# Kernel optimization log

Hardware: AMD Instinct MI355X
Metric: run time of the kernel (lower is better)

Reference implementation:

```python
import jax, jax.numpy as jnp
import numpy as np

N = 8192        # num_nodes
H = 128         # h_dim
E = 131072      # num edges (avg degree 16)
NREL = 90       # num relations
NB = 8          # num_bases (block-diagonal decomposition)
SI = H // NB    # block size 16


def setup_inputs() -> dict:
    key = jax.random.key(0)
    ks = jax.random.split(key, 24)
    sc = 0.01
    n = lambda k, shape, s=sc: jax.random.normal(k, shape, dtype=jnp.float32) * s
    return {
        'node_ids': jnp.arange(N, dtype=jnp.int32),
        'src': jax.random.randint(ks[0], (E,), 0, N, dtype=jnp.int32),
        'dst': jax.random.randint(ks[1], (E,), 0, N, dtype=jnp.int32),
        'etypes': jax.random.randint(ks[2], (E,), 0, NREL, dtype=jnp.int32),
        'norm': jax.random.uniform(ks[3], (E, 1), dtype=jnp.float32),
        'eps': jax.random.normal(ks[4], (N, H), dtype=jnp.float32),
        # input embedding layer
        'embedding': n(ks[5], (N, H)),
        # RelGraphConv layer 0 ('bdd'): per-relation block-diag weights, self-loop, bias
        'W0': n(ks[6], (NREL, NB, SI, SI)),
        'loop0': n(ks[7], (H, H)),
        'b0': jnp.zeros((H,), jnp.float32),
        # RelGraphConv layer 1
        'W1': n(ks[8], (NREL, NB, SI, SI)),
        'loop1': n(ks[9], (H, H)),
        'b1': jnp.zeros((H,), jnp.float32),
        # z_layer: Linear(H, 2H)  (weights stored as (in, out))
        'Wz': n(ks[10], (H, 2 * H)),
        'bz': jnp.zeros((2 * H,), jnp.float32),
        # inter_layer (UpdateLayer): Linear(H, H) + h_bias
        'Wi': n(ks[11], (H, H)),
        'bi': jnp.zeros((H,), jnp.float32),
        'hbi': jnp.zeros((H,), jnp.float32),
        # output_layer (second UpdateLayer)
        'Wo': n(ks[12], (H, H)),
        'bo': jnp.zeros((H,), jnp.float32),
        'hbo': jnp.zeros((H,), jnp.float32),
    }


def _rgcn_bdd(h, W, loop_w, bias, src, dst, etypes, norm, act):
    # gather src features, split into NB blocks of size SI
    x = h[src].reshape(-1, NB, SI)                       # [E, NB, SI]
    Wg = W[etypes]                                       # [E, NB, SI, SI] per-edge relation block weights
    msg = jnp.einsum('ebi,ebio->ebo', x, Wg).reshape(-1, H) * norm  # [E, H]
    agg = jax.ops.segment_sum(msg, dst, num_segments=N)  # scatter-add to dst
    out = agg + bias + h @ loop_w                        # self-loop + bias
    return act(out) if act is not None else out


def reference(node_ids, src, dst, etypes, norm, eps, embedding,
              W0, loop0, b0, W1, loop1, b1,
              Wz, bz, Wi, bi, hbi, Wo, bo, hbo):
    # input layer: embedding lookup; saved as input_embed
    x0 = embedding[node_ids]                             # [N, H]
    h = _rgcn_bdd(x0, W0, loop0, b0, src, dst, etypes, norm, jax.nn.relu)
    h = _rgcn_bdd(h, W1, loop1, b1, src, dst, etypes, norm, None)
    # VAE head: z ~ N(mean, exp(log_std))
    zml = h @ Wz + bz                                    # [N, 2H]
    z_mean, z_log_std = jnp.split(zml, 2, axis=-1)
    z = z_mean + jnp.exp(z_log_std) * eps                # reparameterized sample
    # decode 1: outer-product reconstruction + fused update
    R = z @ z.T                                          # [N, N]
    h = R @ (z @ Wi + bi) + R @ x0 + hbi
    # decode 2
    R2 = h @ h.T                                         # [N, N]
    out = R2 @ (h @ Wo + bo) + R2 @ x0 + hbo
    return out
```

## Files before the change

### kernel.cpp

```cpp
#include <hip/hip_runtime.h>
#include <hip/hip_bf16.h>
#include <math.h>

#define Hdim 128
#define NBq 8
#define SIq 16
#define LDP 136
#define SKX 64

typedef __attribute__((ext_vector_type(8))) short short8x;
typedef __attribute__((ext_vector_type(8))) _Float16 half8x;
typedef __attribute__((ext_vector_type(4))) float f32x4;
typedef __attribute__((ext_vector_type(4))) unsigned short ushort4x;
typedef __attribute__((ext_vector_type(2))) _Float16 half2x;

__device__ inline unsigned short f2b(float f) {
  unsigned int u = __float_as_uint(f);
  return (unsigned short)((u + 0x7fffu + ((u >> 16) & 1u)) >> 16);
}
__device__ inline unsigned int pack2(float lo, float hi) {
  return (unsigned int)f2b(lo) | ((unsigned int)f2b(hi) << 16);
}
__device__ inline unsigned short f2h(float f) {
  _Float16 h = (_Float16)f;
  unsigned short u;
  __builtin_memcpy(&u, &h, 2);
  return u;
}
__device__ inline half2x u2h(unsigned int u) {
  union { unsigned int u; half2x h; } v;
  v.u = u;
  return v.h;
}

__global__ __launch_bounds__(256) void k_pre(
    const float* __restrict__ emb, const int* __restrict__ ids, float* __restrict__ x0,
    unsigned short* __restrict__ x0h, unsigned short* __restrict__ x0t, int Nn,
    const float* __restrict__ W0, unsigned short* __restrict__ Wt0,
    const float* __restrict__ W1, unsigned short* __restrict__ Wt1, int w0elems,
    const float* __restrict__ l0, const float* __restrict__ l1,
    const float* __restrict__ Wi, const float* __restrict__ Wo, const float* __restrict__ Wz,
    unsigned short* __restrict__ l0t, unsigned short* __restrict__ l1t,
    unsigned short* __restrict__ Wit, unsigned short* __restrict__ Wot,
    unsigned short* __restrict__ Wzt,
    const int* __restrict__ dst, int* __restrict__ cnt, int E,
    int b1, int b2, int b3) {
  int bx = blockIdx.x, t = threadIdx.x;
  if (bx < b1) {
    int idx = bx * 256 + t;
    int n = idx >> 5, c4 = idx & 31;
    int s = ids[n];
    float4 v = ((const float4*)emb)[(size_t)s * 32 + c4];
    ((float4*)x0)[(size_t)n * 32 + c4] = v;
    ushort4x h;
    h.x = f2h(v.x); h.y = f2h(v.y); h.z = f2h(v.z); h.w = f2h(v.w);
    ((ushort4x*)x0h)[(size_t)n * 32 + c4] = h;
    int c0 = c4 * 4;
    x0t[(size_t)(c0 + 0) * Nn + n] = h.x;
    x0t[(size_t)(c0 + 1) * Nn + n] = h.y;
    x0t[(size_t)(c0 + 2) * Nn + n] = h.z;
    x0t[(size_t)(c0 + 3) * Nn + n] = h.w;
  } else if (bx < b2) {
    int idx = (bx - b1) * 256 + t;
    const float* W = (idx < w0elems) ? W0 : W1;
    unsigned short* Wt = (idx < w0elems) ? Wt0 : Wt1;
    int local = (idx < w0elems) ? idx : idx - w0elems;
    int rb = local >> 8, io = local & 255;
    int i = io >> 4, o = io & 15;
    Wt[(size_t)rb * 256 + o * 16 + i] = f2h(W[(size_t)rb * 256 + i * 16 + o]);
  } else if (bx < b3) {
    int idx = (bx - b2) * 256 + t;
    if (idx < 65536) {
      int w = idx >> 14, local = idx & 16383;
      const float* in = (w == 0) ? l0 : (w == 1) ? l1 : (w == 2) ? Wi : Wo;
      unsigned short* out = (w == 0) ? l0t : (w == 1) ? l1t : (w == 2) ? Wit : Wot;
      int n = local >> 7, k = local & 127;
      out[local] = f2b(in[k * 128 + n]);
    } else {
      int local = idx - 65536;
      int n = local >> 7, k = local & 127;
      Wzt[local] = f2b(Wz[k * 256 + n]);
    }
  } else {
    int e = (bx - b3) * 256 + t;
    if (e < E) atomicAdd(&cnt[dst[e]], 1);
  }
}

__global__ __launch_bounds__(1024) void k_scan(const int* __restrict__ cnt,
                                               int* __restrict__ off,
                                               int* __restrict__ cur, int N, int E) {
  __shared__ int part[1024];
  int t = threadIdx.x;
  int ipt = N / 1024;
  int base = t * ipt;
  int loc[8];
  int s = 0;
  for (int i = 0; i < ipt; ++i) { loc[i] = s; s += cnt[base + i]; }
  part[t] = s;
  __syncthreads();
  for (int d = 1; d < 1024; d <<= 1) {
    int v = part[t];
    int add = (t >= d) ? part[t - d] : 0;
    __syncthreads();
    part[t] = v + add;
    __syncthreads();
  }
  int pre = (t == 0) ? 0 : part[t - 1];
  for (int i = 0; i < ipt; ++i) {
    int o = pre + loc[i];
    off[base + i] = o;
    cur[base + i] = o;
  }
  if (t == 0) off[N] = E;
}

__global__ void k_scatter(const int* __restrict__ src, const int* __restrict__ dst,
                          const int* __restrict__ et, const float* __restrict__ norm,
                          int* __restrict__ cur, int4* __restrict__ pedge, int E) {
  int e = blockIdx.x * blockDim.x + threadIdx.x;
  if (e >= E) return;
  int p = atomicAdd(&cur[dst[e]], 1);
  pedge[p] = make_int4(src[e], et[e], __float_as_int(norm[e]), 0);
}

__global__ __launch_bounds__(128) void k_edge(
    const unsigned short* __restrict__ xh, const unsigned short* __restrict__ Wt,
    const int* __restrict__ off, const int4* __restrict__ pedge,
    float* __restrict__ agg) {
  int n = blockIdx.x;
  int f = threadIdx.x;
  int b = f >> 4, o = f & 15;
  int j0 = off[n], j1 = off[n + 1];
  float acc = 0.f;
#pragma unroll 2
  for (int j = j0; j < j1; ++j) {
    int4 meta = pedge[j];
    int s = meta.x;
    int r = meta.y;
    float nv = __int_as_float(meta.z);
    const uint4* xp = (const uint4*)(xh + (size_t)s * Hdim + b * SIq);
    const uint4* wp = (const uint4*)(Wt + ((size_t)r * NBq + b) * 256 + o * SIq);
    uint4 xa = xp[0], xc = xp[1];
    uint4 wa = wp[0], wc = wp[1];
#if __has_builtin(__builtin_amdgcn_fdot2)
    float d0 = 0.f, d1 = 0.f;
    d0 = __builtin_amdgcn_fdot2(u2h(xa.x), u2h(wa.x), d0, false);
    d1 = __builtin_amdgcn_fdot2(u2h(xa.y), u2h(wa.y), d1, false);
    d0 = __builtin_amdgcn_fdot2(u2h(xa.z), u2h(wa.z), d0, false);
    d1 = __builtin_amdgcn_fdot2(u2h(xa.w), u2h(wa.w), d1, false);
    d0 = __builtin_amdgcn_fdot2(u2h(xc.x), u2h(wc.x), d0, false);
    d1 = __builtin_amdgcn_fdot2(u2h(xc.y), u2h(wc.y), d1, false);
    d0 = __builtin_amdgcn_fdot2(u2h(xc.z), u2h(wc.z), d0, false);
    d1 = __builtin_amdgcn_fdot2(u2h(xc.w), u2h(wc.w), d1, false);
    acc = fmaf(d0 + d1, nv, acc);
#else
    float d = 0.f;
    unsigned int xu[8] = {xa.x, xa.y, xa.z, xa.w, xc.x, xc.y, xc.z, xc.w};
    unsigned int wu[8] = {wa.x, wa.y, wa.z, wa.w, wc.x, wc.y, wc.z, wc.w};
#pragma unroll
    for (int k = 0; k < 8; ++k) {
      half2x xv = u2h(xu[k]), wv = u2h(wu[k]);
      d += (float)xv.x * (float)wv.x + (float)xv.y * (float)wv.y;
    }
    acc = fmaf(d, nv, acc);
#endif
  }
  agg[(size_t)n * Hdim + f] = acc;
}

__global__ __launch_bounds__(256) void k_bgemm(
    const float* __restrict__ A, const unsigned short* __restrict__ Bt,
    float* __restrict__ C,
    const float* __restrict__ addm, const float* __restrict__ bias,
    int M, int Nc, int relu, unsigned short* __restrict__ Ch) {
  __shared__ unsigned short Al[32][136];
  __shared__ unsigned short Bl[64][136];
  int t = threadIdx.x;
  int bm = blockIdx.x * 32, bn = blockIdx.y * 64;
  {
    int r = t >> 3, c0 = (t & 7) << 4;
    const float4* ap = (const float4*)(A + (size_t)(bm + r) * Hdim + c0);
    float4 a0 = ap[0], a1 = ap[1], a2 = ap[2], a3 = ap[3];
    uint4 p0 = { pack2(a0.x, a0.y), pack2(a0.z, a0.w), pack2(a1.x, a1.y), pack2(a1.z, a1.w) };
    uint4 p1 = { pack2(a2.x, a2.y), pack2(a2.z, a2.w), pack2(a3.x, a3.y), pack2(a3.z, a3.w) };
    *(uint4*)&Al[r][c0]     = p0;
    *(uint4*)&Al[r][c0 + 8] = p1;
  }
  {
    int n = t >> 2, k0 = (t & 3) << 5;
    const uint4* bp = (const uint4*)(Bt + (size_t)(bn + n) * Hdim + k0);
    uint4 b0 = bp[0], b1 = bp[1], b2 = bp[2], b3 = bp[3];
    *(uint4*)&Bl[n][k0]      = b0;
    *(uint4*)&Bl[n][k0 + 8]  = b1;
    *(uint4*)&Bl[n][k0 + 16] = b2;
    *(uint4*)&Bl[n][k0 + 24] = b3;
  }
  __syncthreads();
  int wv = t >> 6, ln = t & 63;
  int mt = wv & 1;
  int nt0 = (wv >> 1) << 1;
  int lm = ln & 15, lk = ln >> 4;
  f32x4 acc0 = {0.f, 0.f, 0.f, 0.f}, acc1 = {0.f, 0.f, 0.f, 0.f};
#pragma unroll
  for (int ks = 0; ks < 4; ++ks) {
    short8x af = *(const short8x*)&Al[mt * 16 + lm][ks * 32 + lk * 8];
    short8x bf0 = *(const short8x*)&Bl[nt0 * 16 + lm][ks * 32 + lk * 8];
    short8x bf1 = *(const short8x*)&Bl[(nt0 + 1) * 16 + lm][ks * 32 + lk * 8];
    acc0 = __builtin_amdgcn_mfma_f32_16x16x32_bf16(af, bf0, acc0, 0, 0, 0);
    acc1 = __builtin_amdgcn_mfma_f32_16x16x32_bf16(af, bf1, acc1, 0, 0, 0);
  }
  int gcol0 = bn + nt0 * 16 + lm;
  int gcol1 = gcol0 + 16;
  float b0v = bias ? bias[gcol0] : 0.f;
  float b1v = bias ? bias[gcol1] : 0.f;
#pragma unroll
  for (int reg = 0; reg < 4; ++reg) {
    int grow = bm + mt * 16 + lk * 4 + reg;
    size_t o0 = (size_t)grow * Nc + gcol0;
    size_t o1 = (size_t)grow * Nc + gcol1;
    float v0 = acc0[reg] + b0v;
    float v1 = acc1[reg] + b1v;
    if (addm) { v0 += addm[o0]; v1 += addm[o1]; }
    if (relu) { v0 = fmaxf(v0, 0.f); v1 = fmaxf(v1, 0.f); }
    C[o0] = v0;
    C[o1] = v1;
    if (Ch) { Ch[o0] = f2h(v0); Ch[o1] = f2h(v1); }
  }
}

__global__ __launch_bounds__(256) void k_bgemm_z(
    const float* __restrict__ A, const unsigned short* __restrict__ Wzt,
    const float* __restrict__ bz, const float* __restrict__ eps,
    float* __restrict__ Z, int M, int Nn,
    unsigned short* __restrict__ Zth, float* __restrict__ gz) {
  __shared__ unsigned short Al[32][136];
  __shared__ unsigned short Bm[64][136];
  __shared__ unsigned short Bl[64][136];
  int t = threadIdx.x;
  int bm = blockIdx.x * 32, bn = blockIdx.y * 64;
  if (gz && blockIdx.x == 0 && blockIdx.y == 0 && t < 64)
    ((float4*)gz)[t] = make_float4(0.f, 0.f, 0.f, 0.f);
  {
    int r = t >> 3, c0 = (t & 7) << 4;
    const float4* ap = (const float4*)(A + (size_t)(bm + r) * Hdim + c0);
    float4 a0 = ap[0], a1 = ap[1], a2 = ap[2], a3 = ap[3];
    uint4 p0 = { pack2(a0.x, a0.y), pack2(a0.z, a0.w), pack2(a1.x, a1.y), pack2(a1.z, a1.w) };
    uint4 p1 = { pack2(a2.x, a2.y), pack2(a2.z, a2.w), pack2(a3.x, a3.y), pack2(a3.z, a3.w) };
    *(uint4*)&Al[r][c0]     = p0;
    *(uint4*)&Al[r][c0 + 8] = p1;
  }
  {
    int n = t >> 2, k0 = (t & 3) << 5;
    const uint4* mp = (const uint4*)(Wzt + (size_t)(bn + n) * Hdim + k0);
    const uint4* lp = (const uint4*)(Wzt + (size_t)(bn + 128 + n) * Hdim + k0);
    uint4 m0 = mp[0], m1 = mp[1], m2 = mp[2], m3 = mp[3];
    uint4 l0 = lp[0], l1 = lp[1], l2 = lp[2], l3 = lp[3];
    *(uint4*)&Bm[n][k0]      = m0; *(uint4*)&Bm[n][k0 + 8]  = m1;
    *(uint4*)&Bm[n][k0 + 16] = m2; *(uint4*)&Bm[n][k0 + 24] = m3;
    *(uint4*)&Bl[n][k0]      = l0; *(uint4*)&Bl[n][k0 + 8]  = l1;
    *(uint4*)&Bl[n][k0 + 16] = l2; *(uint4*)&Bl[n][k0 + 24] = l3;
  }
  __syncthreads();
  int wv = t >> 6, ln = t & 63;
  int mt = wv & 1;
  int nt0 = (wv >> 1) << 1;
  int lm = ln & 15, lk = ln >> 4;
  f32x4 am0 = {0,0,0,0}, am1 = {0,0,0,0}, al0 = {0,0,0,0}, al1 = {0,0,0,0};
#pragma unroll
  for (int ks = 0; ks < 4; ++ks) {
    short8x af = *(const short8x*)&Al[mt * 16 + lm][ks * 32 + lk * 8];
    short8x bm0 = *(const short8x*)&Bm[nt0 * 16 + lm][ks * 32 + lk * 8];
    short8x bm1 = *(const short8x*)&Bm[(nt0 + 1) * 16 + lm][ks * 32 + lk * 8];
    short8x bl0 = *(const short8x*)&Bl[nt0 * 16 + lm][ks * 32 + lk * 8];
    short8x bl1 = *(const short8x*)&Bl[(nt0 + 1) * 16 + lm][ks * 32 + lk * 8];
    am0 = __builtin_amdgcn_mfma_f32_16x16x32_bf16(af, bm0, am0, 0, 0, 0);
    am1 = __builtin_amdgcn_mfma_f32_16x16x32_bf16(af, bm1, am1, 0, 0, 0);
    al0 = __builtin_amdgcn_mfma_f32_16x16x32_bf16(af, bl0, al0, 0, 0, 0);
    al1 = __builtin_amdgcn_mfma_f32_16x16x32_bf16(af, bl1, al1, 0, 0, 0);
  }
  int gcol0 = bn + nt0 * 16 + lm;
  int gcol1 = gcol0 + 16;
  float bm0v = bz[gcol0], bm1v = bz[gcol1];
  float bl0v = bz[128 + gcol0], bl1v = bz[128 + gcol1];
#pragma unroll
  for (int reg = 0; reg < 4; ++reg) {
    int grow = bm + mt * 16 + lk * 4 + reg;
    size_t o0 = (size_t)grow * Hdim + gcol0;
    size_t o1 = (size_t)grow * Hdim + gcol1;
    float v0 = am0[reg] + bm0v + expf(al0[reg] + bl0v) * eps[o0];
    float v1 = am1[reg] + bm1v + expf(al1[reg] + bl1v) * eps[o1];
    Z[o0] = v0;
    Z[o1] = v1;
    Zth[(size_t)gcol0 * Nn + grow] = f2h(v0);
    Zth[(size_t)gcol1 * Nn + grow] = f2h(v1);
  }
}

__global__ __launch_bounds__(256) void k_xty2m(
    const unsigned short* __restrict__ Zt, const unsigned short* __restrict__ X0t,
    float* __restrict__ part, float* __restrict__ s1, float* __restrict__ cx0, int N) {
  int kc = blockIdx.x, yt = blockIdx.y;
  int t = threadIdx.x;
  int KC = N / SKX;
  int k0 = kc * KC;
  if (yt == 4) {
    int c = t & 127;
    const unsigned short* row = ((t >> 7) ? X0t : Zt) + (size_t)c * N + k0;
    float acc = 0.f;
    for (int i = 0; i < KC; i += 8) {
      uint4 v = *(const uint4*)(row + i);
      half2x a0 = u2h(v.x), a1 = u2h(v.y), a2 = u2h(v.z), a3 = u2h(v.w);
      acc += (float)a0.x + (float)a0.y + (float)a1.x + (float)a1.y
           + (float)a2.x + (float)a2.y + (float)a3.x + (float)a3.y;
    }
    atomicAdd(((t >> 7) ? cx0 : s1) + c, acc);
    return;
  }
  __shared__ unsigned short Asl[128][72];
  __shared__ unsigned short Bsl[64][72];
  int wv = t >> 6, ln = t & 63, lm = ln & 15, lk = ln >> 4;
  f32x4 acc[8];
#pragma unroll
  for (int i = 0; i < 8; ++i) acc[i] = (f32x4){0.f, 0.f, 0.f, 0.f};
  for (int ch = 0; ch < KC; ch += 64) {
    {
      int r = t >> 1, s = (t & 1) * 32;
      const uint4* gp = (const uint4*)(Zt + (size_t)r * N + k0 + ch + s);
      uint4 v0 = gp[0], v1 = gp[1], v2 = gp[2], v3 = gp[3];
      *(uint4*)&Asl[r][s]      = v0;
      *(uint4*)&Asl[r][s + 8]  = v1;
      *(uint4*)&Asl[r][s + 16] = v2;
      *(uint4*)&Asl[r][s + 24] = v3;
    }
    if (t < 128) {
      int n = t >> 1, s = (t & 1) * 32;
      int yn = yt * 64 + n;
      const unsigned short* Sb = (yn < 128) ? (Zt + (size_t)yn * N)
                                            : (X0t + (size_t)(yn - 128) * N);
      const uint4* gp = (const uint4*)(Sb + k0 + ch + s);
      uint4 v0 = gp[0], v1 = gp[1], v2 = gp[2], v3 = gp[3];
      *(uint4*)&Bsl[n][s]      = v0;
      *(uint4*)&Bsl[n][s + 8]  = v1;
      *(uint4*)&Bsl[n][s + 16] = v2;
      *(uint4*)&Bsl[n][s + 24] = v3;
    }
    __syncthreads();
#pragma unroll
    for (int ks = 0; ks < 2; ++ks) {
      half8x bf = *(const half8x*)&Bsl[wv * 16 + lm][ks * 32 + lk * 8];
#pragma unroll
      for (int mi = 0; mi < 8; ++mi) {
        half8x af = *(const half8x*)&Asl[mi * 16 + lm][ks * 32 + lk * 8];
        acc[mi] = __builtin_amdgcn_mfma_f32_16x16x32_f16(af, bf, acc[mi], 0, 0, 0);
      }
    }
    __syncthreads();
  }
  int gcol = yt * 64 + wv * 16 + lm;
  float* pb = part + (size_t)kc * (128 * 256) + gcol;
#pragma unroll
  for (int mi = 0; mi < 8; ++mi)
#pragma unroll
    for (int rg = 0; rg < 4; ++rg)
      pb[(size_t)(mi * 16 + lk * 4 + rg) * 256] = acc[mi][rg];
}

__global__ __launch_bounds__(256) void k_red(const float* __restrict__ part,
                                             float* __restrict__ SP) {
  int idx = blockIdx.x * 256 + threadIdx.x;
  float a = 0.f;
#pragma unroll 8
  for (int s = 0; s < SKX; ++s) a += part[(size_t)s * 32768 + idx];
  SP[idx] = a;
}

__device__ inline void stage_f32(unsigned short* dst, const float* __restrict__ src,
                                 int ldF, int t) {
#pragma unroll
  for (int it = 0; it < 2; ++it) {
    int id = it * 1024 + t; int row = id >> 4, ch = id & 15;
    const float4* gp = (const float4*)(src + (size_t)row * ldF) + ch * 2;
    float4 u = gp[0], v = gp[1];
    uint4 pk = { pack2(u.x, u.y), pack2(u.z, u.w), pack2(v.x, v.y), pack2(v.z, v.w) };
    *(uint4*)&dst[row * LDP + ch * 8] = pk;
  }
}
__device__ inline void stage_b16(unsigned short* dst, const unsigned short* __restrict__ src,
                                 int t) {
#pragma unroll
  for (int it = 0; it < 2; ++it) {
    int id = it * 1024 + t; int row = id >> 4, ch = id & 15;
    *(uint4*)&dst[row * LDP + ch * 8] = ((const uint4*)(src + (size_t)row * 128))[ch];
  }
}
__device__ inline void stage_f32T(unsigned short* dst, const float* __restrict__ src,
                                  int ldF, int t) {
#pragma unroll
  for (int it = 0; it < 2; ++it) {
    int id = it * 1024 + t; int n = id >> 4, ig = id & 15;
    unsigned short tmp[8];
#pragma unroll
    for (int u = 0; u < 8; ++u) tmp[u] = f2b(src[(size_t)(ig * 8 + u) * ldF + n]);
    uint4 pk;
    __builtin_memcpy(&pk, tmp, 16);
    *(uint4*)&dst[n * LDP + ig * 8] = pk;
  }
}
__device__ inline void mm128(const unsigned short* A, const unsigned short* B,
                             f32x4 (&Cc)[2][2], int wr, int wc, int lm, int lk) {
#pragma unroll
  for (int ks = 0; ks < 4; ++ks) {
    short8x af0 = *(const short8x*)&A[(wr * 32 + lm) * LDP + ks * 32 + lk * 8];
    short8x af1 = *(const short8x*)&A[(wr * 32 + 16 + lm) * LDP + ks * 32 + lk * 8];
    short8x bf0 = *(const short8x*)&B[(wc * 32 + lm) * LDP + ks * 32 + lk * 8];
    short8x bf1 = *(const short8x*)&B[(wc * 32 + 16 + lm) * LDP + ks * 32 + lk * 8];
    Cc[0][0] = __builtin_amdgcn_mfma_f32_16x16x32_bf16(af0, bf0, Cc[0][0], 0, 0, 0);
    Cc[0][1] = __builtin_amdgcn_mfma_f32_16x16x32_bf16(af0, bf1, Cc[0][1], 0, 0, 0);
    Cc[1][0] = __builtin_amdgcn_mfma_f32_16x16x32_bf16(af1, bf0, Cc[1][0], 0, 0, 0);
    Cc[1][1] = __builtin_amdgcn_mfma_f32_16x16x32_bf16(af1, bf1, Cc[1][1], 0, 0, 0);
  }
}
#define ZEROC {                                           \
  _Pragma("unroll") for (int mi = 0; mi < 2; ++mi)        \
  _Pragma("unroll") for (int ni = 0; ni < 2; ++ni)        \
    C[mi][ni] = (f32x4){0.f, 0.f, 0.f, 0.f}; }
#define CLOOP(body) {                                     \
  _Pragma("unroll") for (int mi = 0; mi < 2; ++mi)        \
  _Pragma("unroll") for (int ni = 0; ni < 2; ++ni)        \
  _Pragma("unroll") for (int rg = 0; rg < 4; ++rg) {      \
    int grow = wr * 32 + mi * 16 + lk * 4 + rg;           \
    int gcol = wc * 32 + ni * 16 + lm;                    \
    float v = C[mi][ni][rg];                              \
    body;                                                 \
  } }

__global__ __launch_bounds__(1024) void k_fix(
    const float* __restrict__ SP, const float* __restrict__ s1g,
    const float* __restrict__ cx0g,
    const unsigned short* __restrict__ Wit, const unsigned short* __restrict__ Wot,
    const float* __restrict__ bi, const float* __restrict__ hbi,
    const float* __restrict__ bo, const float* __restrict__ hbo,
    float* __restrict__ G1g, float* __restrict__ G1tg, float* __restrict__ A2g,
    float* __restrict__ P2g, float* __restrict__ S2g, float* __restrict__ G2tg,
    unsigned short* __restrict__ G12t, float* __restrict__ bvec, float Nf) {
  __shared__ unsigned short Asl[128 * LDP];
  __shared__ unsigned short Bsl[128 * LDP];
  __shared__ float s1l[128], tl[128], s2l[128], cxl[128], bil[128], bol[128], hl[128];
  int t = threadIdx.x;
  int wv = t >> 6, ln = t & 63, lm = ln & 15, lk = ln >> 4;
  int wr = wv >> 2, wc = wv & 3;
  if (t < 128) {
    s1l[t] = s1g[t]; cxl[t] = cx0g[t]; bil[t] = bi[t]; bol[t] = bo[t]; hl[t] = hbi[t];
  }
  f32x4 C[2][2];
  stage_f32(Asl, SP, 256, t);
  stage_b16(Bsl, Wit, t);
  __syncthreads();
  ZEROC; mm128(Asl, Bsl, C, wr, wc, lm, lk);
  CLOOP({
    v += s1l[grow] * bil[gcol] + SP[(size_t)grow * 256 + 128 + gcol];
    G1g[grow * 128 + gcol] = v;
    G1tg[gcol * 128 + grow] = v;
  });
  __syncthreads();
  {
    int row = t >> 3, seg = t & 7;
    const float* gr = G1tg + row * 128 + seg * 16;
    float a2 = 0.f;
#pragma unroll
    for (int i = 0; i < 16; ++i) a2 += gr[i] * s1l[seg * 16 + i];
    a2 += __shfl_xor(a2, 1);
    a2 += __shfl_xor(a2, 2);
    a2 += __shfl_xor(a2, 4);
    if (seg == 0) { tl[row] = a2; s2l[row] = a2 + Nf * hl[row]; }
  }
  __syncthreads();
  stage_f32(Asl, G1tg, 128, t);
  stage_f32(Bsl, SP, 256, t);
  __syncthreads();
  ZEROC; mm128(Asl, Bsl, C, wr, wc, lm, lk);
  CLOOP({ A2g[grow * 128 + gcol] = v; });
  __syncthreads();
  stage_f32T(Bsl, SP + 128, 256, t);
  __syncthreads();
  ZEROC; mm128(Asl, Bsl, C, wr, wc, lm, lk);
  CLOOP({ v += hl[grow] * cxl[gcol]; P2g[grow * 128 + gcol] = v; });
  __syncthreads();
  stage_f32(Asl, A2g, 128, t);
  stage_f32(Bsl, G1tg, 128, t);
  __syncthreads();
  ZEROC; mm128(Asl, Bsl, C, wr, wc, lm, lk);
  CLOOP({
    v += tl[grow] * hl[gcol] + hl[grow] * tl[gcol] + Nf * hl[grow] * hl[gcol];
    S2g[grow * 128 + gcol] = v;
  });
  __syncthreads();
  stage_f32(Asl, S2g, 128, t);
  stage_b16(Bsl, Wot, t);
  __syncthreads();
  ZEROC; mm128(Asl, Bsl, C, wr, wc, lm, lk);
  CLOOP({
    v += s2l[grow] * bol[gcol] + P2g[grow * 128 + gcol];
    G2tg[gcol * 128 + grow] = v;
  });
  __syncthreads();
  stage_f32(Asl, G1g, 128, t);
  stage_f32(Bsl, G2tg, 128, t);
  __syncthreads();
  ZEROC; mm128(Asl, Bsl, C, wr, wc, lm, lk);
  CLOOP({ G12t[gcol * 128 + grow] = f2b(v); });
  __syncthreads();
  {
    int row = t >> 3, seg = t & 7;
    const float* gr = G2tg + row * 128 + seg * 16;
    float a2 = 0.f;
#pragma unroll
    for (int i = 0; i < 16; ++i) a2 += hl[seg * 16 + i] * gr[i];
    a2 += __shfl_xor(a2, 1);
    a2 += __shfl_xor(a2, 2);
    a2 += __shfl_xor(a2, 4);
    if (seg == 0) bvec[row] = a2 + hbo[row];
  }
}

extern "C" void kernel_launch(void* const* d_in, const int* in_sizes, int n_in,
                              void* d_out, int out_size, void* d_ws, size_t ws_size,
                              hipStream_t stream) {
  const int*   node_ids = (const int*)d_in[0];
  const int*   src      = (const int*)d_in[1];
  const int*   dst      = (const int*)d_in[2];
  const int*   et       = (const int*)d_in[3];
  const float* norm     = (const float*)d_in[4];
  const float* eps      = (const float*)d_in[5];
  const float* emb      = (const float*)d_in[6];
  const float* W0       = (const float*)d_in[7];
  const float* loop0    = (const float*)d_in[8];
  const float* b0       = (const float*)d_in[9];
  const float* W1       = (const float*)d_in[10];
  const float* loop1    = (const float*)d_in[11];
  const float* b1       = (const float*)d_in[12];
  const float* Wz       = (const float*)d_in[13];
  const float* bz       = (const float*)d_in[14];
  const float* Wi       = (const float*)d_in[15];
  const float* bi       = (const float*)d_in[16];
  const float* hbi      = (const float*)d_in[17];
  const float* Wo       = (const float*)d_in[18];
  const float* bo       = (const float*)d_in[19];
  const float* hbo      = (const float*)d_in[20];
  float* out = (float*)d_out;

  const int N  = in_sizes[0];
  const int E  = in_sizes[1];
  const int RB = in_sizes[7] / (SIq * SIq);

  char* ws = (char*)d_ws;
  const size_t MB = 1u << 20;
  const size_t KB = 1u << 10;
  float* X0   = (float*)(ws + 0 * MB);
  float* B1p  = (float*)(ws + 4 * MB);
  float* B2p  = (float*)(ws + 8 * MB);
  float* AGG  = (float*)(ws + 12 * MB);
  float* part = (float*)(ws + 8 * MB);
  float* SPb  = (float*)(ws + 16 * MB);
  float* s1p  = SPb + 32768;
  float* cx0p = SPb + 32896;
  float* G1g  = (float*)(ws + 16 * MB + 192 * KB);
  float* G1tg = (float*)(ws + 16 * MB + 256 * KB);
  float* A2g  = (float*)(ws + 16 * MB + 320 * KB);
  float* P2g  = (float*)(ws + 16 * MB + 384 * KB);
  float* S2g  = (float*)(ws + 16 * MB + 448 * KB);
  float* G2tg = (float*)(ws + 16 * MB + 512 * KB);
  unsigned short* G12t = (unsigned short*)(ws + 16 * MB + 576 * KB);
  float* bvec = (float*)(ws + 16 * MB + 640 * KB);
  int*   offp = (int*)(ws + 17 * MB);
  int*   curp = (int*)(ws + 17 * MB + 128 * KB);
  int*   cntp = (int*)(ws + 17 * MB + 256 * KB);
  int4*  pedge = (int4*)(ws + 18 * MB);
  unsigned short* Wt0 = (unsigned short*)(ws + 20 * MB);
  unsigned short* Wt1 = (unsigned short*)(ws + 20 * MB + 512 * KB);
  unsigned short* l0t = (unsigned short*)(ws + 21 * MB);
  unsigned short* l1t = (unsigned short*)(ws + 21 * MB + 64 * KB);
  unsigned short* Wit = (unsigned short*)(ws + 21 * MB + 128 * KB);
  unsigned short* Wot = (unsigned short*)(ws + 21 * MB + 192 * KB);
  unsigned short* Wzt = (unsigned short*)(ws + 21 * MB + 256 * KB);
  unsigned short* X0H = (unsigned short*)(ws + 22 * MB);
  unsigned short* B1H = (unsigned short*)(ws + 24 * MB);
  unsigned short* Ztc = (unsigned short*)(ws + 26 * MB);
  unsigned short* X0t = (unsigned short*)(ws + 28 * MB);

  dim3 blk(256);

  const int w0elems = RB * 256;
  const int gB   = (N * 32) / 256;
  const int wtbB = (2 * w0elems + 255) / 256;
  const int wttB = 98304 / 256;
  const int histB = (E + 255) / 256;
  const int b1s = gB, b2s = gB + wtbB, b3s = gB + wtbB + wttB;
  hipMemsetAsync(cntp, 0, (size_t)N * sizeof(int), stream);
  k_pre<<<dim3(b3s + histB), blk, 0, stream>>>(
      emb, node_ids, X0, X0H, X0t, N, W0, Wt0, W1, Wt1, w0elems,
      loop0, loop1, Wi, Wo, Wz, l0t, l1t, Wit, Wot, Wzt,
      dst, cntp, E, b1s, b2s, b3s);
  k_scan<<<dim3(1), dim3(1024), 0, stream>>>(cntp, offp, curp, N, E);
  k_scatter<<<dim3((E + 255) / 256), blk, 0, stream>>>(src, dst, et, norm, curp, pedge, E);

  k_edge<<<dim3(N), dim3(128), 0, stream>>>(X0H, Wt0, offp, pedge, AGG);
  k_bgemm<<<dim3(N / 32, 2), blk, 0, stream>>>(X0, l0t, B1p, AGG, b0, N, Hdim, 1, B1H);
  k_edge<<<dim3(N), dim3(128), 0, stream>>>(B1H, Wt1, offp, pedge, AGG);
  k_bgemm<<<dim3(N / 32, 2), blk, 0, stream>>>(B1p, l1t, B2p, AGG, b1, N, Hdim, 0, nullptr);
  k_bgemm_z<<<dim3(N / 32, 2), blk, 0, stream>>>(B2p, Wzt, bz, eps, B1p, N, N, Ztc, s1p);
  k_xty2m<<<dim3(SKX, 5), blk, 0, stream>>>(Ztc, X0t, part, s1p, cx0p, N);
  k_red<<<dim3(128), blk, 0, stream>>>(part, SPb);
  k_fix<<<dim3(1), dim3(1024), 0, stream>>>(SPb, s1p, cx0p, Wit, Wot, bi, hbi, bo, hbo,
                                            G1g, G1tg, A2g, P2g, S2g, G2tg, G12t, bvec,
                                            (float)N);
  k_bgemm<<<dim3(N / 32, 2), blk, 0, stream>>>(B1p, G12t, out, nullptr, bvec, N, Hdim, 0, nullptr);
}
```

Baseline: 270.7 us.

## Keep k_fix intermediates in LDS as bf16 instead of global fp32 round-trips

The single-block k_fix kernel used to write each 128x128 intermediate (G1, G1^T, A2, P2, S2, G2^T) to global memory in fp32 and re-stage it into LDS with bf16 conversion. The rewrite keeps these matrices resident in four LDS tiles in bf16, reusing transposed layouts so later MFMA stages read them directly. This is meant to remove global traffic and staging latency from a serial one-block kernel. In exchange it uses more LDS (about 139KB), and intermediates such as P2 and the G1^T reduction now pass through bf16 instead of fp32, which could cost some accuracy.

```diff
diff --git a/kernel.cpp b/kernel.cpp
--- a/kernel.cpp
+++ b/kernel.cpp
@@ -31,6 +31,9 @@
   union { unsigned int u; half2x h; } v;
   v.u = u;
   return v.h;
+}
+__device__ inline float b2f(unsigned short u) {
+  return __uint_as_float(((unsigned int)u) << 16);
 }
 
 __global__ __launch_bounds__(256) void k_pre(
@@ -394,19 +397,6 @@
     *(uint4*)&dst[row * LDP + ch * 8] = ((const uint4*)(src + (size_t)row * 128))[ch];
   }
 }
-__device__ inline void stage_f32T(unsigned short* dst, const float* __restrict__ src,
-                                  int ldF, int t) {
-#pragma unroll
-  for (int it = 0; it < 2; ++it) {
-    int id = it * 1024 + t; int n = id >> 4, ig = id & 15;
-    unsigned short tmp[8];
-#pragma unroll
-    for (int u = 0; u < 8; ++u) tmp[u] = f2b(src[(size_t)(ig * 8 + u) * ldF + n]);
-    uint4 pk;
-    __builtin_memcpy(&pk, tmp, 16);
-    *(uint4*)&dst[n * LDP + ig * 8] = pk;
-  }
-}
 __device__ inline void mm128(const unsigned short* A, const unsigned short* B,
                              f32x4 (&Cc)[2][2], int wr, int wc, int lm, int lk) {
 #pragma unroll
@@ -425,15 +415,6 @@
   _Pragma("unroll") for (int mi = 0; mi < 2; ++mi)        \
   _Pragma("unroll") for (int ni = 0; ni < 2; ++ni)        \
     C[mi][ni] = (f32x4){0.f, 0.f, 0.f, 0.f}; }
-#define CLOOP(body) {                                     \
-  _Pragma("unroll") for (int mi = 0; mi < 2; ++mi)        \
-  _Pragma("unroll") for (int ni = 0; ni < 2; ++ni)        \
-  _Pragma("unroll") for (int rg = 0; rg < 4; ++rg) {      \
-    int grow = wr * 32 + mi * 16 + lk * 4 + rg;           \
-    int gcol = wc * 32 + ni * 16 + lm;                    \
-    float v = C[mi][ni][rg];                              \
-    body;                                                 \
-  } }
 
 __global__ __launch_bounds__(1024) void k_fix(
     const float* __restrict__ SP, const float* __restrict__ s1g,
@@ -441,11 +422,11 @@
     const unsigned short* __restrict__ Wit, const unsigned short* __restrict__ Wot,
     const float* __restrict__ bi, const float* __restrict__ hbi,
     const float* __restrict__ bo, const float* __restrict__ hbo,
-    float* __restrict__ G1g, float* __restrict__ G1tg, float* __restrict__ A2g,
-    float* __restrict__ P2g, float* __restrict__ S2g, float* __restrict__ G2tg,
     unsigned short* __restrict__ G12t, float* __restrict__ bvec, float Nf) {
-  __shared__ unsigned short Asl[128 * LDP];
-  __shared__ unsigned short Bsl[128 * LDP];
+  __shared__ unsigned short T0[128 * LDP];
+  __shared__ unsigned short T1[128 * LDP];
+  __shared__ unsigned short T2[128 * LDP];
+  __shared__ unsigned short T3[128 * LDP];
   __shared__ float s1l[128], tl[128], s2l[128], cxl[128], bil[128], bol[128], hl[128];
   int t = threadIdx.x;
   int wv = t >> 6, ln = t & 63, lm = ln & 15, lk = ln >> 4;
@@ -453,74 +434,154 @@
   if (t < 128) {
     s1l[t] = s1g[t]; cxl[t] = cx0g[t]; bil[t] = bi[t]; bol[t] = bo[t]; hl[t] = hbi[t];
   }
+  stage_f32(T0, SP, 256, t);
+  stage_b16(T1, Wit, t);
+  __syncthreads();
   f32x4 C[2][2];
-  stage_f32(Asl, SP, 256, t);
-  stage_b16(Bsl, Wit, t);
-  __syncthreads();
-  ZEROC; mm128(Asl, Bsl, C, wr, wc, lm, lk);
-  CLOOP({
-    v += s1l[grow] * bil[gcol] + SP[(size_t)grow * 256 + 128 + gcol];
-    G1g[grow * 128 + gcol] = v;
-    G1tg[gcol * 128 + grow] = v;
-  });
+  ZEROC; mm128(T0, T1, C, wr, wc, lm, lk);
+#pragma unroll
+  for (int mi = 0; mi < 2; ++mi)
+#pragma unroll
+  for (int ni = 0; ni < 2; ++ni) {
+    int gcol = wc * 32 + ni * 16 + lm;
+    int g0 = wr * 32 + mi * 16 + lk * 4;
+    ushort4x pk;
+#pragma unroll
+    for (int rg = 0; rg < 4; ++rg) {
+      int grow = g0 + rg;
+      float v = C[mi][ni][rg] + s1l[grow] * bil[gcol] + SP[(size_t)grow * 256 + 128 + gcol];
+      unsigned short hv = f2b(v);
+      T2[grow * LDP + gcol] = hv;
+      pk[rg] = hv;
+    }
+    *(ushort4x*)&T3[gcol * LDP + g0] = pk;
+  }
   __syncthreads();
   {
     int row = t >> 3, seg = t & 7;
-    const float* gr = G1tg + row * 128 + seg * 16;
+    const unsigned short* gr = T3 + row * LDP + seg * 16;
     float a2 = 0.f;
 #pragma unroll
-    for (int i = 0; i < 16; ++i) a2 += gr[i] * s1l[seg * 16 + i];
+    for (int i = 0; i < 16; ++i) a2 += b2f(gr[i]) * s1l[seg * 16 + i];
     a2 += __shfl_xor(a2, 1);
     a2 += __shfl_xor(a2, 2);
     a2 += __shfl_xor(a2, 4);
     if (seg == 0) { tl[row] = a2; s2l[row] = a2 + Nf * hl[row]; }
   }
   __syncthreads();
-  stage_f32(Asl, G1tg, 128, t);
-  stage_f32(Bsl, SP, 256, t);
-  __syncthreads();
-  ZEROC; mm128(Asl, Bsl, C, wr, wc, lm, lk);
-  CLOOP({ A2g[grow * 128 + gcol] = v; });
-  __syncthreads();
-  stage_f32T(Bsl, SP + 128, 256, t);
-  __syncthreads();
-  ZEROC; mm128(Asl, Bsl, C, wr, wc, lm, lk);
-  CLOOP({ v += hl[grow] * cxl[gcol]; P2g[grow * 128 + gcol] = v; });
-  __syncthreads();
-  stage_f32(Asl, A2g, 128, t);
-  stage_f32(Bsl, G1tg, 128, t);
-  __syncthreads();
-  ZEROC; mm128(Asl, Bsl, C, wr, wc, lm, lk);
-  CLOOP({
-    v += tl[grow] * hl[gcol] + hl[grow] * tl[gcol] + Nf * hl[grow] * hl[gcol];
-    S2g[grow * 128 + gcol] = v;
-  });
-  __syncthreads();
-  stage_f32(Asl, S2g, 128, t);
-  stage_b16(Bsl, Wot, t);
-  __syncthreads();
-  ZEROC; mm128(Asl, Bsl, C, wr, wc, lm, lk);
-  CLOOP({
-    v += s2l[grow] * bol[gcol] + P2g[grow * 128 + gcol];
-    G2tg[gcol * 128 + grow] = v;
-  });
-  __syncthreads();
-  stage_f32(Asl, G1g, 128, t);
-  stage_f32(Bsl, G2tg, 128, t);
-  __syncthreads();
-  ZEROC; mm128(Asl, Bsl, C, wr, wc, lm, lk);
-  CLOOP({ G12t[gcol * 128 + grow] = f2b(v); });
+  ZEROC; mm128(T3, T0, C, wr, wc, lm, lk);
+  __syncthreads();
+#pragma unroll
+  for (int mi = 0; mi < 2; ++mi)
+#pragma unroll
+  for (int ni = 0; ni < 2; ++ni) {
+    int gcol = wc * 32 + ni * 16 + lm;
+    int g0 = wr * 32 + mi * 16 + lk * 4;
+#pragma unroll
+    for (int rg = 0; rg < 4; ++rg)
+      T1[(g0 + rg) * LDP + gcol] = f2b(C[mi][ni][rg]);
+  }
+  {
+#pragma unroll
+    for (int it = 0; it < 2; ++it) {
+      int id = it * 1024 + t; int row = id >> 4, c0 = (id & 15) * 8;
+      const float4* gp = (const float4*)(SP + (size_t)row * 256 + 128 + c0);
+      float4 u = gp[0], v2 = gp[1];
+      float vals[8] = {u.x, u.y, u.z, u.w, v2.x, v2.y, v2.z, v2.w};
+#pragma unroll
+      for (int q = 0; q < 8; ++q) T0[(c0 + q) * LDP + row] = f2b(vals[q]);
+    }
+  }
+  __syncthreads();
+  ZEROC; mm128(T3, T0, C, wr, wc, lm, lk);
+  __syncthreads();
+#pragma unroll
+  for (int mi = 0; mi < 2; ++mi)
+#pragma unroll
+  for (int ni = 0; ni < 2; ++ni) {
+    int gcol = wc * 32 + ni * 16 + lm;
+    int g0 = wr * 32 + mi * 16 + lk * 4;
+#pragma unroll
+    for (int rg = 0; rg < 4; ++rg) {
+      int grow = g0 + rg;
+      T0[grow * LDP + gcol] = f2b(C[mi][ni][rg] + hl[grow] * cxl[gcol]);
+    }
+  }
+  __syncthreads();
+  ZEROC; mm128(T1, T3, C, wr, wc, lm, lk);
+  __syncthreads();
+#pragma unroll
+  for (int mi = 0; mi < 2; ++mi)
+#pragma unroll
+  for (int ni = 0; ni < 2; ++ni) {
+    int gcol = wc * 32 + ni * 16 + lm;
+    int g0 = wr * 32 + mi * 16 + lk * 4;
+#pragma unroll
+    for (int rg = 0; rg < 4; ++rg) {
+      int grow = g0 + rg;
+      float v = C[mi][ni][rg] + tl[grow] * hl[gcol] + hl[grow] * tl[gcol]
+              + Nf * hl[grow] * hl[gcol];
+      T1[grow * LDP + gcol] = f2b(v);
+    }
+  }
+  stage_b16(T3, Wot, t);
+  __syncthreads();
+  ZEROC; mm128(T1, T3, C, wr, wc, lm, lk);
+  float g2v[2][2][4];
+#pragma unroll
+  for (int mi = 0; mi < 2; ++mi)
+#pragma unroll
+  for (int ni = 0; ni < 2; ++ni) {
+    int gcol = wc * 32 + ni * 16 + lm;
+    int g0 = wr * 32 + mi * 16 + lk * 4;
+#pragma unroll
+    for (int rg = 0; rg < 4; ++rg) {
+      int grow = g0 + rg;
+      g2v[mi][ni][rg] = C[mi][ni][rg] + s2l[grow] * bol[gcol]
+                      + b2f(T0[grow * LDP + gcol]);
+    }
+  }
+  __syncthreads();
+#pragma unroll
+  for (int mi = 0; mi < 2; ++mi)
+#pragma unroll
+  for (int ni = 0; ni < 2; ++ni) {
+    int gcol = wc * 32 + ni * 16 + lm;
+    int g0 = wr * 32 + mi * 16 + lk * 4;
+    ushort4x pk;
+#pragma unroll
+    for (int rg = 0; rg < 4; ++rg) pk[rg] = f2b(g2v[mi][ni][rg]);
+    *(ushort4x*)&T0[gcol * LDP + g0] = pk;
+  }
   __syncthreads();
   {
     int row = t >> 3, seg = t & 7;
-    const float* gr = G2tg + row * 128 + seg * 16;
+    const unsigned short* gr = T0 + row * LDP + seg * 16;
     float a2 = 0.f;
 #pragma unroll
-    for (int i = 0; i < 16; ++i) a2 += hl[seg * 16 + i] * gr[i];
+    for (int i = 0; i < 16; ++i) a2 += hl[seg * 16 + i] * b2f(gr[i]);
     a2 += __shfl_xor(a2, 1);
     a2 += __shfl_xor(a2, 2);
     a2 += __shfl_xor(a2, 4);
     if (seg == 0) bvec[row] = a2 + hbo[row];
+  }
+  ZEROC; mm128(T2, T0, C, wr, wc, lm, lk);
+#pragma unroll
+  for (int mi = 0; mi < 2; ++mi)
+#pragma unroll
+  for (int ni = 0; ni < 2; ++ni) {
+    int gcol = wc * 32 + ni * 16 + lm;
+    int g0 = wr * 32 + mi * 16 + lk * 4;
+    ushort4x pk;
+#pragma unroll
+    for (int rg = 0; rg < 4; ++rg) pk[rg] = f2b(C[mi][ni][rg]);
+    *(ushort4x*)&T1[gcol * LDP + g0] = pk;
+  }
+  __syncthreads();
+#pragma unroll
+  for (int it = 0; it < 2; ++it) {
+    int id = it * 1024 + t; int row = id >> 4, ch = (id & 15) * 8;
+    *(uint4*)&G12t[row * 128 + ch] = *(uint4*)&T1[row * LDP + ch];
   }
 }
 
@@ -565,12 +626,6 @@
   float* SPb  = (float*)(ws + 16 * MB);
   float* s1p  = SPb + 32768;
   float* cx0p = SPb + 32896;
-  float* G1g  = (float*)(ws + 16 * MB + 192 * KB);
-  float* G1tg = (float*)(ws + 16 * MB + 256 * KB);
-  float* A2g  = (float*)(ws + 16 * MB + 320 * KB);
-  float* P2g  = (float*)(ws + 16 * MB + 384 * KB);
-  float* S2g  = (float*)(ws + 16 * MB + 448 * KB);
-  float* G2tg = (float*)(ws + 16 * MB + 512 * KB);
   unsigned short* G12t = (unsigned short*)(ws + 16 * MB + 576 * KB);
   float* bvec = (float*)(ws + 16 * MB + 640 * KB);
   int*   offp = (int*)(ws + 17 * MB);
@@ -613,7 +668,6 @@
   k_xty2m<<<dim3(SKX, 5), blk, 0, stream>>>(Ztc, X0t, part, s1p, cx0p, N);
   k_red<<<dim3(128), blk, 0, stream>>>(part, SPb);
   k_fix<<<dim3(1), dim3(1024), 0, stream>>>(SPb, s1p, cx0p, Wit, Wot, bi, hbi, bo, hbo,
-                                            G1g, G1tg, A2g, P2g, S2g, G2tg, G12t, bvec,
-                                            (float)N);
+                                            G12t, bvec, (float)N);
   k_bgemm<<<dim3(N / 32, 2), blk, 0, stream>>>(B1p, G12t, out, nullptr, bvec, N, Hdim, 0, nullptr);
 }
```

After: 253.2 us. 6.5% less time.
